# Kernel tuning notes

Measured on AMD Instinct MI355X. Metric: run time of the kernel, lower is better.

## Reference

```python
import jax, jax.numpy as jnp
import numpy as np
import math

IN_C, OUT_C = 64, 128
OUT_C1 = int((OUT_C - IN_C) * 0.3 + IN_C)  # 83
OUT_C2 = int((OUT_C - IN_C) * 0.6 + IN_C)  # 102
OUT_C3 = OUT_C                              # 128
RESIDUE_RATIO = 0.5
R_RES = math.sqrt(RESIDUE_RATIO)
R_SC = math.sqrt(1.0 - RESIDUE_RATIO)
PRELU_INIT = 0.25
POST_MEAN = (1.0 - PRELU_INIT) / math.sqrt(2.0 * math.pi)
_POST_EX2 = (1.0 + PRELU_INIT ** 2) / 2.0
POST_STDV = math.sqrt(_POST_EX2 - POST_MEAN ** 2)


def _conv1x1_weight(key, out_c, in_c):
    # torch Conv1d custom init: normal_, then divide by per-out-channel L2 norm
    w = jax.random.normal(key, (out_c, in_c), dtype=jnp.float32)
    norm = jnp.sqrt(jnp.sum(w ** 2, axis=1, keepdims=True) + 1e-8)
    return w / norm


def cprelu(x, w):
    # x: [B, C, N], w: [C]
    y = jnp.where(x >= 0, x, x * w[None, :, None])
    return (y - POST_MEAN) / POST_STDV


def setup_inputs() -> dict:
    key = jax.random.key(0)
    ks = jax.random.split(key, 8)
    x = jax.random.normal(ks[0], (16, IN_C, 8192), dtype=jnp.float32)
    conn = jax.random.uniform(ks[1], (4096, 8192), dtype=jnp.float32)
    return {
        "x": x,
        "conn": conn,
        "w1": _conv1x1_weight(ks[2], OUT_C1, IN_C),
        "b1": jnp.zeros((OUT_C1,), jnp.float32),
        "p1": jnp.full((OUT_C1,), PRELU_INIT, jnp.float32),
        "w2": _conv1x1_weight(ks[3], OUT_C2, OUT_C1),
        "b2": jnp.zeros((OUT_C2,), jnp.float32),
        "p2": jnp.full((OUT_C2,), PRELU_INIT, jnp.float32),
        "wm": _conv1x1_weight(ks[4], OUT_C3, OUT_C2),
        "bm": jnp.zeros((OUT_C3,), jnp.float32),
        "p3": jnp.full((OUT_C3,), PRELU_INIT, jnp.float32),
        "ws": _conv1x1_weight(ks[5], OUT_C, IN_C),
        "bs": jnp.zeros((OUT_C,), jnp.float32),
    }


def _forward(x, conn, w1, b1, p1, w2, b2, p2, wm, bm, p3, ws, bs):
    # self-connection matrix: binary mask of per-row argmax entries (ties kept)
    sc = (conn - jnp.max(conn, axis=1, keepdims=True) >= 0).astype(jnp.float32)

    # residue branch: 1x1 conv -> CPReLU -> 1x1 conv -> CPReLU -> Meshconv -> CPReLU
    h = cprelu(jnp.einsum('bcn,oc->bon', x, w1) + b1[None, :, None], p1)
    h = cprelu(jnp.einsum('bcn,oc->bon', h, w2) + b2[None, :, None], p2)
    h = jnp.einsum('bcn,oc->bon', h, wm) + bm[None, :, None]      # [B, C3, Nin]
    h = jnp.einsum('oi,bci->bco', conn, h)                         # mesh pooling -> [B, C3, Nout]
    res = cprelu(h, p3)

    # shortcut branch: Meshconv with self_connection_matrix (1x1 conv + pooled gather)
    s = jnp.einsum('bcn,oc->bon', x, ws) + bs[None, :, None]       # [B, OUT_C, Nin]
    s = jnp.einsum('oi,bci->bco', sc, s)                           # [B, OUT_C, Nout]

    return s * R_SC + res * R_RES


def reference(x, conn, w1, b1, p1, w2, b2, p2, wm, bm, p3, ws, bs):
    return _forward(x, conn, w1, b1, p1, w2, b2, p2, wm, bm, p3, ws, bs)
```

## Files before the change

### kernel.cpp

```cpp
#include <hip/hip_runtime.h>
#include <hip/hip_bf16.h>
#include <stdint.h>

using bf16x8 = __attribute__((ext_vector_type(8))) __bf16;
using bf16x4 = __attribute__((ext_vector_type(4))) __bf16;
using f32x4  = __attribute__((ext_vector_type(4))) float;

typedef const uint32_t __attribute__((address_space(1)))* gas_ptr;
typedef uint32_t __attribute__((address_space(3)))* las_ptr;

__device__ __forceinline__ void load_lds16(const void* g, void* l) {
    __builtin_amdgcn_global_load_lds((gas_ptr)g, (las_ptr)l, 16, 0, 0);
}

#define PM  0.29920671030107454f
#define PIS 1.5046096f
#define RHALF 0.70710678118654752f

__global__ __launch_bounds__(256) void k_prep(const float* __restrict__ w1,
                                              const float* __restrict__ w2,
                                              const float* __restrict__ wm,
                                              const float* __restrict__ wsw,
                                              __bf16* __restrict__ W1p,
                                              __bf16* __restrict__ W2p,
                                              __bf16* __restrict__ WMp,
                                              __bf16* __restrict__ WSp)
{
    const int id = blockIdx.x * 256 + threadIdx.x;
    const int stride = gridDim.x * 256;
    for (int i = id; i < 96 * 64; i += stride) {
        int oc = i >> 6, ic = i & 63;
        W1p[i] = (__bf16)((oc < 83) ? w1[oc * 64 + ic] : 0.f);
    }
    for (int i = id; i < 112 * 96; i += stride) {
        int oc = i / 96, ic = i % 96;
        W2p[i] = (__bf16)((oc < 102 && ic < 83) ? w2[oc * 83 + ic] : 0.f);
    }
    for (int i = id; i < 128 * 128; i += stride) {
        int oc = i >> 7, ic = i & 127;
        WMp[i] = (__bf16)((ic < 102) ? wm[oc * 102 + ic] : 0.f);
    }
    for (int i = id; i < 128 * 64; i += stride) {
        WSp[i] = (__bf16)wsw[i];
    }
}

template<int KS>
__device__ __forceinline__ f32x4 mfma_tile(const __bf16* __restrict__ W, int wstride, int mt,
                                           const __bf16* B, int bstride, int nt, int lane)
{
    f32x4 acc = {0.f, 0.f, 0.f, 0.f};
    const int l15 = lane & 15;
    const int kg  = (lane >> 4) << 3;
    const __bf16* wp = W + (mt * 16 + l15) * wstride + kg;
    const __bf16* bp = B + (nt * 16 + l15) * bstride + kg;
#pragma unroll
    for (int ks = 0; ks < KS; ks++) {
        bf16x8 av = *(const bf16x8*)(wp + ks * 32);
        bf16x8 bv = *(const bf16x8*)(bp + ks * 32);
        acc = __builtin_amdgcn_mfma_f32_16x16x32_bf16(av, bv, acc, 0, 0, 0);
    }
    return acc;
}

__global__ __launch_bounds__(256) void k_cc(
    const float* __restrict__ conn, __bf16* __restrict__ cb, size_t rowstride,
    int* __restrict__ cnt, int* __restrict__ idx,
    const float* __restrict__ x,
    const float* __restrict__ b1, const float* __restrict__ p1,
    const float* __restrict__ b2, const float* __restrict__ p2,
    const float* __restrict__ bm, const float* __restrict__ bs,
    const __bf16* __restrict__ W1p, const __bf16* __restrict__ W2p,
    const __bf16* __restrict__ WMp, const __bf16* __restrict__ WSp,
    __bf16* __restrict__ h3, __bf16* __restrict__ s_t)
{
    __shared__ __align__(16) char pool[38528];
    const int t = threadIdx.x;
    const int bx = blockIdx.x;
    const int r3 = bx % 3;
    const int g  = bx / 3;

    if (r3 < 2) {
        const int o = 2 * g + r3;
        float* wmax = (float*)pool;
        int*   scnt = (int*)(pool + 16);
        const float* row = conn + (size_t)o * 8192;
        float4 v[8];
        float m = -1e30f;
#pragma unroll
        for (int q = 0; q < 8; q++) {
            v[q] = *(const float4*)(row + (size_t)(q * 256 + t) * 4);
            m = fmaxf(m, fmaxf(fmaxf(v[q].x, v[q].y), fmaxf(v[q].z, v[q].w)));
        }
        __syncthreads();
        __bf16* drow = cb + (size_t)o * rowstride;
#pragma unroll
        for (int q = 0; q < 8; q++) {
            bf16x4 w;
            w[0] = (__bf16)v[q].x; w[1] = (__bf16)v[q].y;
            w[2] = (__bf16)v[q].z; w[3] = (__bf16)v[q].w;
            *(bf16x4*)(drow + (size_t)(q * 256 + t) * 4) = w;
        }
#pragma unroll
        for (int off = 32; off > 0; off >>= 1) m = fmaxf(m, __shfl_down(m, off, 64));
        if ((t & 63) == 0) wmax[t >> 6] = m;
        if (t == 0) *scnt = 0;
        __syncthreads();
        const float rmax = fmaxf(fmaxf(wmax[0], wmax[1]), fmaxf(wmax[2], wmax[3]));
#pragma unroll
        for (int q = 0; q < 8; q++) {
            float vv[4] = {v[q].x, v[q].y, v[q].z, v[q].w};
#pragma unroll
            for (int e = 0; e < 4; e++) {
                if (vv[e] >= rmax) {
                    int p = atomicAdd(scnt, 1);
                    if (p < 16) idx[o * 16 + p] = (q * 256 + t) * 4 + e;
                }
            }
        }
        __syncthreads();
        if (t == 0) cnt[o] = *scnt < 16 ? *scnt : 16;
        return;
    }

    const int b  = g >> 7;
    const int p0 = (g & 127) * 64;
    __bf16* buf0 = (__bf16*)pool;
    __bf16* un   = (__bf16*)(pool + 17408);
    float*  bl   = (float*)(pool + 35840);
    __bf16* St   = un;
    __bf16* H1t  = un;
    __bf16* OutT = un;
    float* b1l = bl;       float* p1l = bl + 96;
    float* b2l = bl + 192; float* p2l = bl + 304;
    float* bml = bl + 416; float* bsl = bl + 544;

    const int lane = t & 63, wid = t >> 6;

    for (int i = t; i < 96; i += 256)  { b1l[i] = (i < 83)  ? b1[i] : 0.f; p1l[i] = (i < 83)  ? p1[i] : 0.f; }
    for (int i = t; i < 112; i += 256) { b2l[i] = (i < 102) ? b2[i] : 0.f; p2l[i] = (i < 102) ? p2[i] : 0.f; }
    for (int i = t; i < 128; i += 256) { bml[i] = bm[i]; bsl[i] = bs[i]; }

    {
        const int pg = (t & 15) * 4;
        const int c0 = t >> 4;
#pragma unroll
        for (int it = 0; it < 4; it++) {
            int c = it * 16 + c0;
            float4 xv = *(const float4*)(x + ((size_t)b * 64 + c) * 8192 + p0 + pg);
            buf0[(pg + 0) * 72 + c] = (__bf16)xv.x;
            buf0[(pg + 1) * 72 + c] = (__bf16)xv.y;
            buf0[(pg + 2) * 72 + c] = (__bf16)xv.z;
            buf0[(pg + 3) * 72 + c] = (__bf16)xv.w;
        }
    }
    __syncthreads();

    const int quad4 = (lane >> 4) << 2;
    const int l15 = lane & 15;

    for (int tt = wid; tt < 32; tt += 4) {
        int mt = tt >> 2, nt = tt & 3;
        f32x4 a = mfma_tile<2>(WSp, 64, mt, buf0, 72, nt, lane);
        int ocb = mt * 16 + quad4;
        int pos = nt * 16 + l15;
        bf16x4 ov;
#pragma unroll
        for (int r = 0; r < 4; r++) ov[r] = (__bf16)(a[r] + bsl[ocb + r]);
        *(bf16x4*)(&St[pos * 136 + ocb]) = ov;
    }
    __syncthreads();

#pragma unroll
    for (int it = 0; it < 4; it++) {
        int lin = it * 256 + t;
        int pos = lin >> 4, pc = lin & 15;
        bf16x8 v = *(const bf16x8*)(&St[pos * 136 + pc * 8]);
        *(bf16x8*)(s_t + ((size_t)b * 8192 + p0 + pos) * 128 + pc * 8) = v;
    }
    __syncthreads();

    for (int tt = wid; tt < 24; tt += 4) {
        int mt = tt >> 2, nt = tt & 3;
        f32x4 a = mfma_tile<2>(W1p, 64, mt, buf0, 72, nt, lane);
        int ocb = mt * 16 + quad4;
        int pos = nt * 16 + l15;
        bf16x4 ov;
#pragma unroll
        for (int r = 0; r < 4; r++) {
            float v = a[r] + b1l[ocb + r];
            v = (v >= 0.f) ? v : v * p1l[ocb + r];
            ov[r] = (__bf16)((v - PM) * PIS);
        }
        *(bf16x4*)(&H1t[pos * 104 + ocb]) = ov;
    }
    __syncthreads();

    for (int tt = wid; tt < 28; tt += 4) {
        int mt = tt >> 2, nt = tt & 3;
        f32x4 a = mfma_tile<3>(W2p, 96, mt, H1t, 104, nt, lane);
        int ocb = mt * 16 + quad4;
        int pos = nt * 16 + l15;
        bf16x4 ov;
#pragma unroll
        for (int r = 0; r < 4; r++) {
            float v = a[r] + b2l[ocb + r];
            v = (v >= 0.f) ? v : v * p2l[ocb + r];
            ov[r] = (__bf16)((v - PM) * PIS);
        }
        *(bf16x4*)(&buf0[pos * 136 + ocb]) = ov;
    }
    for (int i = t; i < 64 * 16; i += 256) {
        int pos = i >> 4, c = 112 + (i & 15);
        buf0[pos * 136 + c] = (__bf16)0.f;
    }
    __syncthreads();

    for (int tt = wid; tt < 32; tt += 4) {
        int mt = tt >> 2, nt = tt & 3;
        f32x4 a = mfma_tile<4>(WMp, 128, mt, buf0, 136, nt, lane);
        int ocb = mt * 16 + quad4;
        int pos = nt * 16 + l15;
#pragma unroll
        for (int r = 0; r < 4; r++)
            OutT[(ocb + r) * 72 + pos] = (__bf16)(a[r] + bml[ocb + r]);
    }
    __syncthreads();

#pragma unroll
    for (int it = 0; it < 4; it++) {
        int lin = it * 256 + t;
        int ch = lin >> 3, pc = lin & 7;
        bf16x8 v = *(const bf16x8*)(OutT + ch * 72 + pc * 8);
        *(bf16x8*)(h3 + ((size_t)b * 128 + ch) * 8192 + p0 + pc * 8) = v;
    }
}

__global__ __launch_bounds__(256, 2) void k_gemm(const __bf16* __restrict__ A,
                                                 const __bf16* __restrict__ B,
                                                 size_t bstride,
                                                 float* __restrict__ out,
                                                 const __bf16* __restrict__ s_t,
                                                 const int* __restrict__ idx,
                                                 const int* __restrict__ cnt,
                                                 const float* __restrict__ p3)
{
    __shared__ __align__(16) char pool[66560];
    __bf16* la = (__bf16*)pool;
    __bf16* lb = (__bf16*)(pool + 16384);
    float*  sp = (float*)pool;
    float* p3l = (float*)(pool + 66048);

    const int t = threadIdx.x;
    const int lane = t & 63;
    const int wid = t >> 6;
    const int tMi = blockIdx.y;
    const int tM = tMi * 128;
    const int tN = blockIdx.x * 128;
    const int wm2 = (wid & 1) * 64;
    const int wn2 = (wid >> 1) * 64;

    f32x4 acc[4][4];
    const f32x4 zero = {0.f, 0.f, 0.f, 0.f};
#pragma unroll
    for (int i = 0; i < 4; i++)
#pragma unroll
        for (int j = 0; j < 4; j++) acc[i][j] = zero;

    const int tr = t >> 3;
    const int sc = (t & 7) ^ (tr & 7);
    const __bf16* pA[4];
    const __bf16* pB[4];
#pragma unroll
    for (int i = 0; i < 4; i++) {
        pA[i] = A + (size_t)(tM + i * 32 + tr) * 8192 + sc * 8;
        pB[i] = B + (size_t)(tN + i * 32 + tr) * bstride + sc * 8;
    }

    const int l15 = lane & 15;
    const int q = lane >> 4;
    int aoff[4], boff[4];
#pragma unroll
    for (int i = 0; i < 4; i++) {
        int row = wm2 + i * 16 + l15;
        aoff[i] = row * 64 + ((q ^ (row & 7)) * 8);
    }
#pragma unroll
    for (int j = 0; j < 4; j++) {
        int row = wn2 + j * 16 + l15;
        boff[j] = row * 64 + ((q ^ (row & 7)) * 8);
    }

    for (int it = 0; it < 128; it++) {
#pragma unroll
        for (int i = 0; i < 4; i++) load_lds16(pA[i], la + (i * 256 + t) * 8);
#pragma unroll
        for (int i = 0; i < 4; i++) load_lds16(pB[i], lb + (i * 256 + t) * 8);
#pragma unroll
        for (int i = 0; i < 4; i++) { pA[i] += 64; pB[i] += 64; }
        __syncthreads();
#pragma unroll
        for (int ks = 0; ks < 2; ks++) {
            bf16x8 af[4], bfr[4];
#pragma unroll
            for (int i = 0; i < 4; i++) af[i]  = *(const bf16x8*)(la + (aoff[i] ^ (ks << 5)));
#pragma unroll
            for (int j = 0; j < 4; j++) bfr[j] = *(const bf16x8*)(lb + (boff[j] ^ (ks << 5)));
#pragma unroll
            for (int i = 0; i < 4; i++)
#pragma unroll
                for (int j = 0; j < 4; j++)
                    acc[i][j] = __builtin_amdgcn_mfma_f32_16x16x32_bf16(af[i], bfr[j], acc[i][j], 0, 0, 0);
        }
        __syncthreads();
    }

    {
        const int l = t >> 1;
        const int part = t & 1;
        const int col = tN + l;
        const int n = cnt[col];
        const __bf16* base = s_t + ((size_t)tMi * 8192) * 128 + part * 64;
        float* spr = sp + l * 129 + part * 64;
        {
            const __bf16* row = base + (size_t)idx[col * 16] * 128;
#pragma unroll
            for (int j = 0; j < 8; j++) {
                bf16x8 v = *(const bf16x8*)(row + j * 8);
#pragma unroll
                for (int u = 0; u < 8; u++) spr[j * 8 + u] = (float)v[u];
            }
        }
        for (int k = 1; k < n; k++) {
            const __bf16* row = base + (size_t)idx[col * 16 + k] * 128;
#pragma unroll
            for (int j = 0; j < 8; j++) {
                bf16x8 v = *(const bf16x8*)(row + j * 8);
#pragma unroll
                for (int u = 0; u < 8; u++) spr[j * 8 + u] += (float)v[u];
            }
        }
        if (t < 128) p3l[t] = p3[t];
    }
    __syncthreads();

    const int quad4 = q * 4;
#pragma unroll
    for (int i = 0; i < 4; i++) {
        int gm = tM + wm2 + i * 16 + quad4;
#pragma unroll
        for (int j = 0; j < 4; j++) {
            int gn = tN + wn2 + j * 16 + l15;
            int colT = wn2 + j * 16 + l15;
#pragma unroll
            for (int r = 0; r < 4; r++) {
                int c = wm2 + i * 16 + quad4 + r;
                float v = acc[i][j][r];
                float pw = p3l[c];
                float y = (v >= 0.f) ? v : v * pw;
                y = (y - PM) * PIS;
                out[(size_t)(gm + r) * 4096 + gn] = sp[colT * 129 + c] * RHALF + y * RHALF;
            }
        }
    }
}

extern "C" void kernel_launch(void* const* d_in, const int* in_sizes, int n_in,
                              void* d_out, int out_size, void* d_ws, size_t ws_size,
                              hipStream_t stream) {
    (void)in_sizes; (void)n_in; (void)out_size;
    const float* x    = (const float*)d_in[0];
    const float* conn = (const float*)d_in[1];
    const float* w1   = (const float*)d_in[2];
    const float* b1   = (const float*)d_in[3];
    const float* p1   = (const float*)d_in[4];
    const float* w2   = (const float*)d_in[5];
    const float* b2   = (const float*)d_in[6];
    const float* p2   = (const float*)d_in[7];
    const float* wm   = (const float*)d_in[8];
    const float* bm   = (const float*)d_in[9];
    const float* p3   = (const float*)d_in[10];
    const float* wsw  = (const float*)d_in[11];
    const float* bs   = (const float*)d_in[12];
    float* out = (float*)d_out;

    char* ws = (char*)d_ws;
    __bf16* h3  = (__bf16*)(ws);
    __bf16* s_t = (__bf16*)(ws + 33554432);
    __bf16* W1p = (__bf16*)(ws + 67108864);
    __bf16* W2p = (__bf16*)(ws + 67108864 + 12288);
    __bf16* WMp = (__bf16*)(ws + 67108864 + 33792);
    __bf16* WSp = (__bf16*)(ws + 67108864 + 66560);
    int* idx = (int*)(ws + 67108864 + 82944);
    int* cnt = (int*)(ws + 67108864 + 82944 + 262144);
    const size_t connb_off = 67108864 + 82944 + 262144 + 16384;

    __bf16* connb;
    size_t  cstride;
    if (ws_size >= connb_off + (size_t)4096 * 8192 * 2) {
        connb = (__bf16*)(ws + connb_off);
        cstride = 8192;
    } else {
        connb = (__bf16*)const_cast<float*>(conn);
        cstride = 16384;
    }

    k_prep<<<32, 256, 0, stream>>>(w1, w2, wm, wsw, W1p, W2p, WMp, WSp);
    k_cc<<<6144, 256, 0, stream>>>(conn, connb, cstride, cnt, idx,
                                   x, b1, p1, b2, p2, bm, bs,
                                   W1p, W2p, WMp, WSp, h3, s_t);
    k_gemm<<<dim3(32, 16), 256, 0, stream>>>(h3, connb, cstride, out, s_t, idx, cnt, p3);
}
```

Measured before the change: 465.2 us.

## Split GEMM K dimension across two wave groups within each block

The main GEMM block grows from 256 to 512 threads. Each half of the block handles half of the 8192-long K dimension in its own LDS buffers, and the two partial accumulators are merged through shared memory before the epilogue. The shortcut gather is also spread over four threads per column instead of two. The aim is more waves per CU to hide load and MFMA latency on the 512-block grid. The cost is an extra LDS reduction and sync, half the threads sitting idle in the epilogue, and higher register pressure under the new launch bounds.

```diff
diff --git a/kernel.cpp b/kernel.cpp
--- a/kernel.cpp
+++ b/kernel.cpp
@@ -236,7 +236,7 @@
     }
 }
 
-__global__ __launch_bounds__(256, 2) void k_gemm(const __bf16* __restrict__ A,
+__global__ __launch_bounds__(512, 4) void k_gemm(const __bf16* __restrict__ A,
                                                  const __bf16* __restrict__ B,
                                                  size_t bstride,
                                                  float* __restrict__ out,
@@ -246,19 +246,22 @@
                                                  const float* __restrict__ p3)
 {
     __shared__ __align__(16) char pool[66560];
-    __bf16* la = (__bf16*)pool;
-    __bf16* lb = (__bf16*)(pool + 16384);
-    float*  sp = (float*)pool;
+    float* sp  = (float*)pool;
     float* p3l = (float*)(pool + 66048);
 
     const int t = threadIdx.x;
     const int lane = t & 63;
     const int wid = t >> 6;
+    const int q4 = wid & 3;
+    const int h  = wid >> 2;
     const int tMi = blockIdx.y;
     const int tM = tMi * 128;
     const int tN = blockIdx.x * 128;
-    const int wm2 = (wid & 1) * 64;
-    const int wn2 = (wid >> 1) * 64;
+    const int wm2 = (q4 & 1) * 64;
+    const int wn2 = (q4 >> 1) * 64;
+
+    __bf16* la = (__bf16*)pool + h * 16384;
+    __bf16* lb = la + 8192;
 
     f32x4 acc[4][4];
     const f32x4 zero = {0.f, 0.f, 0.f, 0.f};
@@ -267,14 +270,18 @@
 #pragma unroll
         for (int j = 0; j < 4; j++) acc[i][j] = zero;
 
-    const int tr = t >> 3;
-    const int sc = (t & 7) ^ (tr & 7);
+    const int hs = t >> 8;
+    const int tl = t & 255;
+    const int tr = tl >> 3;
+    const int sc = (tl & 7) ^ (tr & 7);
+    __bf16* sla = (__bf16*)pool + hs * 16384;
+    __bf16* slb = sla + 8192;
     const __bf16* pA[4];
     const __bf16* pB[4];
 #pragma unroll
     for (int i = 0; i < 4; i++) {
-        pA[i] = A + (size_t)(tM + i * 32 + tr) * 8192 + sc * 8;
-        pB[i] = B + (size_t)(tN + i * 32 + tr) * bstride + sc * 8;
+        pA[i] = A + (size_t)(tM + i * 32 + tr) * 8192 + hs * 4096 + sc * 8;
+        pB[i] = B + (size_t)(tN + i * 32 + tr) * bstride + hs * 4096 + sc * 8;
     }
 
     const int l15 = lane & 15;
@@ -291,11 +298,11 @@
         boff[j] = row * 64 + ((q ^ (row & 7)) * 8);
     }
 
-    for (int it = 0; it < 128; it++) {
-#pragma unroll
-        for (int i = 0; i < 4; i++) load_lds16(pA[i], la + (i * 256 + t) * 8);
-#pragma unroll
-        for (int i = 0; i < 4; i++) load_lds16(pB[i], lb + (i * 256 + t) * 8);
+    for (int it = 0; it < 64; it++) {
+#pragma unroll
+        for (int i = 0; i < 4; i++) load_lds16(pA[i], sla + (i * 256 + tl) * 8);
+#pragma unroll
+        for (int i = 0; i < 4; i++) load_lds16(pB[i], slb + (i * 256 + tl) * 8);
 #pragma unroll
         for (int i = 0; i < 4; i++) { pA[i] += 64; pB[i] += 64; }
         __syncthreads();
@@ -315,17 +322,38 @@
         __syncthreads();
     }
 
+    float* mrg = (float*)pool;
+    if (h == 1) {
+#pragma unroll
+        for (int i = 0; i < 4; i++)
+#pragma unroll
+            for (int j = 0; j < 4; j++)
+                *(f32x4*)(mrg + q4 * 4096 + (i * 4 + j) * 256 + lane * 4) = acc[i][j];
+    }
+    __syncthreads();
+    if (h == 0) {
+#pragma unroll
+        for (int i = 0; i < 4; i++)
+#pragma unroll
+            for (int j = 0; j < 4; j++) {
+                f32x4 m = *(const f32x4*)(mrg + q4 * 4096 + (i * 4 + j) * 256 + lane * 4);
+#pragma unroll
+                for (int r = 0; r < 4; r++) acc[i][j][r] += m[r];
+            }
+    }
+    __syncthreads();
+
     {
-        const int l = t >> 1;
-        const int part = t & 1;
+        const int l = t >> 2;
+        const int part = t & 3;
         const int col = tN + l;
         const int n = cnt[col];
-        const __bf16* base = s_t + ((size_t)tMi * 8192) * 128 + part * 64;
-        float* spr = sp + l * 129 + part * 64;
+        const __bf16* base = s_t + ((size_t)tMi * 8192) * 128 + part * 32;
+        float* spr = sp + l * 129 + part * 32;
         {
             const __bf16* row = base + (size_t)idx[col * 16] * 128;
 #pragma unroll
-            for (int j = 0; j < 8; j++) {
+            for (int j = 0; j < 4; j++) {
                 bf16x8 v = *(const bf16x8*)(row + j * 8);
 #pragma unroll
                 for (int u = 0; u < 8; u++) spr[j * 8 + u] = (float)v[u];
@@ -334,7 +362,7 @@
         for (int k = 1; k < n; k++) {
             const __bf16* row = base + (size_t)idx[col * 16 + k] * 128;
 #pragma unroll
-            for (int j = 0; j < 8; j++) {
+            for (int j = 0; j < 4; j++) {
                 bf16x8 v = *(const bf16x8*)(row + j * 8);
 #pragma unroll
                 for (int u = 0; u < 8; u++) spr[j * 8 + u] += (float)v[u];
@@ -344,22 +372,24 @@
     }
     __syncthreads();
 
-    const int quad4 = q * 4;
-#pragma unroll
-    for (int i = 0; i < 4; i++) {
-        int gm = tM + wm2 + i * 16 + quad4;
-#pragma unroll
-        for (int j = 0; j < 4; j++) {
-            int gn = tN + wn2 + j * 16 + l15;
-            int colT = wn2 + j * 16 + l15;
-#pragma unroll
-            for (int r = 0; r < 4; r++) {
-                int c = wm2 + i * 16 + quad4 + r;
-                float v = acc[i][j][r];
-                float pw = p3l[c];
-                float y = (v >= 0.f) ? v : v * pw;
-                y = (y - PM) * PIS;
-                out[(size_t)(gm + r) * 4096 + gn] = sp[colT * 129 + c] * RHALF + y * RHALF;
+    if (h == 0) {
+        const int quad4 = q * 4;
+#pragma unroll
+        for (int i = 0; i < 4; i++) {
+            int gm = tM + wm2 + i * 16 + quad4;
+#pragma unroll
+            for (int j = 0; j < 4; j++) {
+                int gn = tN + wn2 + j * 16 + l15;
+                int colT = wn2 + j * 16 + l15;
+#pragma unroll
+                for (int r = 0; r < 4; r++) {
+                    int c = wm2 + i * 16 + quad4 + r;
+                    float v = acc[i][j][r];
+                    float pw = p3l[c];
+                    float y = (v >= 0.f) ? v : v * pw;
+                    y = (y - PM) * PIS;
+                    out[(size_t)(gm + r) * 4096 + gn] = sp[colT * 129 + c] * RHALF + y * RHALF;
+                }
             }
         }
     }
@@ -409,5 +439,5 @@
     k_cc<<<6144, 256, 0, stream>>>(conn, connb, cstride, cnt, idx,
                                    x, b1, p1, b2, p2, bm, bs,
                                    W1p, W2p, WMp, WSp, h3, s_t);
-    k_gemm<<<dim3(32, 16), 256, 0, stream>>>(h3, connb, cstride, out, s_t, idx, cnt, p3);
-}
+    k_gemm<<<dim3(32, 16), 512, 0, stream>>>(h3, connb, cstride, out, s_t, idx, cnt, p3);
+}
```

Result: slower. 553.0 us (+18.9%).
